# Kernel tuning notes

Hardware: AMD Instinct MI355X
Metric: run time of the kernel (lower is better)

Reference implementation:

```python
import jax, jax.numpy as jnp
import numpy as np

B, T, K = 128, 512, 256  # batch, seq_len, num_tags


def setup_inputs() -> dict:
    key = jax.random.key(0)
    k1, k2, k3 = jax.random.split(key, 3)
    y_pred = jax.random.normal(k1, (B, T, K), dtype=jnp.float32)
    trans = jax.random.normal(k2, (K, K), dtype=jnp.float32)
    y_true = jax.random.randint(k3, (B, T), 0, K)
    return {"y_pred": y_pred, "trans": trans, "y_true": y_true}


def reference(y_pred, trans, y_true):
    # sparse_loss: one-hot the integer labels
    num_tags = trans.shape[0]
    y_oh = jax.nn.one_hot(y_true, num_tags, dtype=y_pred.dtype)  # [B,T,K]

    # dense_loss: mask frames where all logits <= -1e6
    mask = jnp.all(y_pred > -1e6, axis=2, keepdims=True).astype(y_pred.dtype)  # [B,T,1]
    y_oh = y_oh * mask
    yp = y_pred * mask

    # target_score: emission score + transition score along the gold path
    point_score = jnp.einsum('bti,bti->b', y_oh, yp)
    trans_score = jnp.einsum('bti,ij,btj->b', y_oh[:, :-1], trans, y_oh[:, 1:])
    target_score = point_score + trans_score  # [B]

    # log_norm_step: forward algorithm (log-semiring recurrence) via scan
    init = yp[:, 0]  # [B,K]

    def step(alpha, xm):
        x, m = xm  # x: [B,K] emissions at t, m: [B,1] mask at t
        # logsumexp over previous tag: alpha[b,i] + trans[i,j]
        new = jax.nn.logsumexp(alpha[:, :, None] + trans[None, :, :], axis=1) + x
        alpha = m * new + (1.0 - m) * alpha
        return alpha, None

    xs = (jnp.swapaxes(yp[:, 1:], 0, 1), jnp.swapaxes(mask[:, 1:], 0, 1))  # time-major
    last_alpha, _ = jax.lax.scan(step, init, xs)  # [B,K]
    log_norm = jax.nn.logsumexp(last_alpha, axis=1)  # [B]

    return log_norm - target_score  # per-example CRF negative log-likelihood [B]
```

## Files before the change

kernel.cpp:

```cpp
#include <hip/hip_runtime.h>
#include <stdint.h>

#define T_ 512
#define K_ 256
#define NB 16
#define L2E 1.4426950408889634f
#define LN2 0.6931471805599453f

typedef __attribute__((ext_vector_type(8))) short short8;
typedef __attribute__((ext_vector_type(4))) float f32x4;

__device__ __forceinline__ float fexp2(float x) {
#if __has_builtin(__builtin_amdgcn_exp2f)
  return __builtin_amdgcn_exp2f(x);
#else
  return exp2f(x);
#endif
}
__device__ __forceinline__ float flog2(float x) {
#if __has_builtin(__builtin_amdgcn_logf)
  return __builtin_amdgcn_logf(x);
#else
  return log2f(x);
#endif
}
__device__ __forceinline__ unsigned int umax_(unsigned int a, unsigned int b) {
  return a > b ? a : b;
}
__device__ __forceinline__ unsigned short f2bf(float f) {
  union { float f; uint32_t u; } v; v.f = f;
  uint32_t r = v.u + 0x7fffu + ((v.u >> 16) & 1u);
  return (unsigned short)(r >> 16);
}

#define BAR() do { \
  asm volatile("s_waitcnt lgkmcnt(0)" ::: "memory"); \
  __builtin_amdgcn_s_barrier(); \
  asm volatile("" ::: "memory"); \
} while (0)


__global__ void prep_E(const float* __restrict__ trans, unsigned short* __restrict__ Efrag) {
  int idx = blockIdx.x * 256 + threadIdx.x;
  int e = idx & 7;
  int ln = (idx >> 3) & 63;
  int kb = (idx >> 9) & 7;
  int mt = idx >> 12;
  int j = mt * 16 + (ln & 15);
  int k = kb * 32 + ((ln >> 4) << 3) + e;
  Efrag[idx] = f2bf(__expf(trans[k * K_ + j]));
}

__global__ void aux_mask(const float* __restrict__ yp, unsigned char* __restrict__ masks) {
  int item = blockIdx.x * 4 + (threadIdx.x >> 6);
  int lane = threadIdx.x & 63;
  const float4 v = *(const float4*)(yp + (size_t)item * K_ + lane * 4);
  float mn = fminf(fminf(v.x, v.y), fminf(v.z, v.w));
  unsigned long long bl = __ballot(mn > -1000000.0f);
  if (lane == 0) {
    int b = item >> 9, t = item & 511;
    masks[t * 128 + b] = (bl == ~0ull) ? 1 : 0;
  }
}

__global__ void aux_score(const float* __restrict__ yp, const float* __restrict__ trans,
                          const int* __restrict__ ytrue, const unsigned char* __restrict__ masks,
                          float* __restrict__ score) {
  int b = blockIdx.x;
  int lane = threadIdx.x;
  float s = 0.f;
  #pragma unroll
  for (int k = 0; k < 8; ++k) {
    int t = lane + 64 * k;
    int y = ytrue[b * T_ + t];
    int m = masks[t * 128 + b];
    float x = yp[((size_t)b * T_ + t) * K_ + y];
    if (m) s += x;
    if (t >= 1) {
      int ym = ytrue[b * T_ + t - 1];
      int mm = masks[(t - 1) * 128 + b];
      if (m && mm) s += trans[ym * K_ + y];
    }
  }
  #pragma unroll
  for (int off = 32; off; off >>= 1) s += __shfl_xor(s, off, 64);
  if (lane == 0) score[b] = s;
}


template<int TM4, bool RESC, bool MWR, bool MASKED>
__device__ __forceinline__ void crf_step(
    int t, int c, int g, int wv, int swz, const int* tb,
    const short8 (&Ef)[4][8],
    float (&a)[16], float (&exf)[16], int& acc, int& mkc,
    const float* xb, float4 (&XN)[4], float4 (&XI)[4],
    unsigned short (*Wl)[NB * K_], const unsigned char* mkl, unsigned int* Mpart) {
  BAR();
  if (RESC) {
    unsigned int Mx = Mpart[c];
    Mx = umax_(Mx, Mpart[NB + c]);
    Mx = umax_(Mx, Mpart[2 * NB + c]);
    Mx = umax_(Mx, Mpart[3 * NB + c]);
    unsigned int e_ = Mx >> 23;
    float sf = __builtin_bit_cast(float, (254u - e_) << 23);
    if (!MASKED || mkc) acc += 127 - (int)e_;
    #pragma unroll
    for (int j = 0; j < 16; ++j) exf[j] *= sf;
  }
  f32x4 ac0 = {0.f, 0.f, 0.f, 0.f}, ac1 = {0.f, 0.f, 0.f, 0.f};
  f32x4 ac2 = {0.f, 0.f, 0.f, 0.f}, ac3 = {0.f, 0.f, 0.f, 0.f};
  {
    const unsigned short* rrow = &Wl[TM4 & 1][c * K_];
    #pragma unroll
    for (int kb = 0; kb < 8; ++kb) {
      short8 bf = __builtin_bit_cast(short8,
          *(const uint4*)(&rrow[(kb * 32 + g * 8) ^ swz]));
      ac0 = __builtin_amdgcn_mfma_f32_16x16x32_bf16(Ef[0][kb], bf, ac0, 0, 0, 0);
      ac1 = __builtin_amdgcn_mfma_f32_16x16x32_bf16(Ef[1][kb], bf, ac1, 0, 0, 0);
      ac2 = __builtin_amdgcn_mfma_f32_16x16x32_bf16(Ef[2][kb], bf, ac2, 0, 0, 0);
      ac3 = __builtin_amdgcn_mfma_f32_16x16x32_bf16(Ef[3][kb], bf, ac3, 0, 0, 0);
    }
  }
  if (MASKED) {
    #pragma unroll
    for (int i = 0; i < 4; ++i) { float an = ac0[i] * exf[i];      a[i]      = mkc ? an : a[i]; }
    #pragma unroll
    for (int i = 0; i < 4; ++i) { float an = ac1[i] * exf[4 + i];  a[4 + i]  = mkc ? an : a[4 + i]; }
    #pragma unroll
    for (int i = 0; i < 4; ++i) { float an = ac2[i] * exf[8 + i];  a[8 + i]  = mkc ? an : a[8 + i]; }
    #pragma unroll
    for (int i = 0; i < 4; ++i) { float an = ac3[i] * exf[12 + i]; a[12 + i] = mkc ? an : a[12 + i]; }
  } else {
    #pragma unroll
    for (int i = 0; i < 4; ++i) a[i]      = ac0[i] * exf[i];
    #pragma unroll
    for (int i = 0; i < 4; ++i) a[4 + i]  = ac1[i] * exf[4 + i];
    #pragma unroll
    for (int i = 0; i < 4; ++i) a[8 + i]  = ac2[i] * exf[8 + i];
    #pragma unroll
    for (int i = 0; i < 4; ++i) a[12 + i] = ac3[i] * exf[12 + i];
  }
  {
    unsigned short* wrow = &Wl[(TM4 + 1) & 1][c * K_];
    #pragma unroll
    for (int m = 0; m < 4; ++m) {
      uint32_t p0 = __builtin_amdgcn_perm(
          __builtin_bit_cast(uint32_t, a[4 * m + 1]),
          __builtin_bit_cast(uint32_t, a[4 * m + 0]), 0x07060302u);
      uint32_t p1 = __builtin_amdgcn_perm(
          __builtin_bit_cast(uint32_t, a[4 * m + 3]),
          __builtin_bit_cast(uint32_t, a[4 * m + 2]), 0x07060302u);
      uint2 pp; pp.x = p0; pp.y = p1;
      *(uint2*)(&wrow[tb[m] ^ swz]) = pp;
    }
  }
  if (MWR) {
    unsigned int pm = __builtin_bit_cast(uint32_t, a[0]);
    #pragma unroll
    for (int j = 1; j < 16; ++j) pm = umax_(pm, __builtin_bit_cast(uint32_t, a[j]));
    pm = umax_(pm, (unsigned int)__shfl_xor((int)pm, 16, 64));
    pm = umax_(pm, (unsigned int)__shfl_xor((int)pm, 32, 64));
    if (g == 0) Mpart[wv * NB + c] = pm;
  }
  #pragma unroll
  for (int m = 0; m < 4; ++m) {
    exf[4 * m + 0] = fexp2(XN[m].x * L2E);
    exf[4 * m + 1] = fexp2(XN[m].y * L2E);
    exf[4 * m + 2] = fexp2(XN[m].z * L2E);
    exf[4 * m + 3] = fexp2(XN[m].w * L2E);
  }
  if (MASKED) mkc = mkl[(t + 1 < T_ ? t + 1 : 0) * NB + c];
  {
    int tt = t + 4;
    tt = tt > (T_ - 1) ? (T_ - 1) : tt;
    #pragma unroll
    for (int m = 0; m < 4; ++m)
      XI[m] = *(const float4*)(xb + (size_t)tt * K_ + tb[m]);
  }
}

template<bool MASKED>
__device__ __forceinline__ void scan_run(
    int tid, int c, int g, int wv, int swz, const int* tb, int b0,
    const short8 (&Ef)[4][8], const float* xb,
    float4 (&xinit)[4], float4 (&X0q)[4], float4 (&X1q)[4],
    float4 (&X2q)[4], float4 (&X3q)[4],
    unsigned short (*Wl)[NB * K_], const unsigned char* mkl,
    unsigned int* Mpart, float* Spart,
    const float* __restrict__ score, float* __restrict__ out) {
  float a[16], exf[16];
  int acc = 0;
  int mkc = 0;
  {
    int mk0 = MASKED ? mkl[c] : 1;
    #pragma unroll
    for (int m = 0; m < 4; ++m) {
      float e0 = fexp2(xinit[m].x * L2E);
      float e1 = fexp2(xinit[m].y * L2E);
      float e2 = fexp2(xinit[m].z * L2E);
      float e3 = fexp2(xinit[m].w * L2E);
      a[4 * m + 0] = (MASKED && !mk0) ? 1.0f : e0;
      a[4 * m + 1] = (MASKED && !mk0) ? 1.0f : e1;
      a[4 * m + 2] = (MASKED && !mk0) ? 1.0f : e2;
      a[4 * m + 3] = (MASKED && !mk0) ? 1.0f : e3;
    }
  }
  {
    unsigned short* wrow = &Wl[1][c * K_];
    #pragma unroll
    for (int m = 0; m < 4; ++m) {
      uint32_t p0 = __builtin_amdgcn_perm(
          __builtin_bit_cast(uint32_t, a[4 * m + 1]),
          __builtin_bit_cast(uint32_t, a[4 * m + 0]), 0x07060302u);
      uint32_t p1 = __builtin_amdgcn_perm(
          __builtin_bit_cast(uint32_t, a[4 * m + 3]),
          __builtin_bit_cast(uint32_t, a[4 * m + 2]), 0x07060302u);
      uint2 pp; pp.x = p0; pp.y = p1;
      *(uint2*)(&wrow[tb[m] ^ swz]) = pp;
    }
  }
  #pragma unroll
  for (int m = 0; m < 4; ++m) {
    exf[4 * m + 0] = fexp2(X1q[m].x * L2E);
    exf[4 * m + 1] = fexp2(X1q[m].y * L2E);
    exf[4 * m + 2] = fexp2(X1q[m].z * L2E);
    exf[4 * m + 3] = fexp2(X1q[m].w * L2E);
  }
  if (MASKED) mkc = mkl[NB + c];

  crf_step<1, false, false, MASKED>(1, c, g, wv, swz, tb, Ef, a, exf, acc, mkc, xb, X2q, X1q, Wl, mkl, Mpart);
  crf_step<2, false, false, MASKED>(2, c, g, wv, swz, tb, Ef, a, exf, acc, mkc, xb, X3q, X2q, Wl, mkl, Mpart);
  crf_step<3, false, true , MASKED>(3, c, g, wv, swz, tb, Ef, a, exf, acc, mkc, xb, X0q, X3q, Wl, mkl, Mpart);

  #pragma unroll 1
  for (int t0 = 4; t0 < T_; t0 += 4) {
    crf_step<0, true , false, MASKED>(t0,     c, g, wv, swz, tb, Ef, a, exf, acc, mkc, xb, X1q, X0q, Wl, mkl, Mpart);
    crf_step<1, false, false, MASKED>(t0 + 1, c, g, wv, swz, tb, Ef, a, exf, acc, mkc, xb, X2q, X1q, Wl, mkl, Mpart);
    crf_step<2, false, false, MASKED>(t0 + 2, c, g, wv, swz, tb, Ef, a, exf, acc, mkc, xb, X3q, X2q, Wl, mkl, Mpart);
    crf_step<3, false, true , MASKED>(t0 + 3, c, g, wv, swz, tb, Ef, a, exf, acc, mkc, xb, X0q, X3q, Wl, mkl, Mpart);
  }

  __syncthreads();
  {
    float ssum = 0.f;
    #pragma unroll
    for (int j = 0; j < 16; ++j) ssum += a[j];
    ssum += __shfl_xor(ssum, 16, 64);
    ssum += __shfl_xor(ssum, 32, 64);
    if (g == 0) Spart[wv * NB + c] = ssum;
  }
  __syncthreads();
  if (tid < NB) {
    float S = Spart[tid] + Spart[NB + tid] + Spart[2 * NB + tid] + Spart[3 * NB + tid];
    out[b0 + tid] = LN2 * (flog2(S) - (float)acc) - score[b0 + tid];
  }
}

__global__ __launch_bounds__(256, 1) void crf_scan(
    const float* __restrict__ yp, const unsigned short* __restrict__ Efrag,
    const unsigned char* __restrict__ masks, const float* __restrict__ score,
    float* __restrict__ out) {
  const int b0 = blockIdx.x * NB;
  const int tid = threadIdx.x;
  const int wv = tid >> 6, lane = tid & 63;
  const int c = lane & 15;
  const int g = lane >> 4;
  const int swz = (c & 7) << 3;

  __shared__ unsigned short Wl[2][NB * K_];
  __shared__ unsigned char mkl[T_ * NB];
  __shared__ unsigned int Mpart[4 * NB];
  __shared__ float Spart[4 * NB];
  __shared__ int sflag[4];

  short8 Ef[4][8];
  {
    const uint4* ep = (const uint4*)Efrag;
    #pragma unroll
    for (int m = 0; m < 4; ++m)
      #pragma unroll
      for (int kb = 0; kb < 8; ++kb)
        Ef[m][kb] = __builtin_bit_cast(short8, ep[((wv * 4 + m) * 8 + kb) * 64 + lane]);
  }

  uint4 md0, md1;
  {
    uint4* dst = (uint4*)mkl;
    md0 = *(const uint4*)(masks + (tid)*128 + b0);
    md1 = *(const uint4*)(masks + (tid + 256) * 128 + b0);
    dst[tid] = md0;
    dst[tid + 256] = md1;
  }

  const float* xb = yp + (size_t)(b0 + c) * T_ * K_;
  int tb[4];
  #pragma unroll
  for (int m = 0; m < 4; ++m) tb[m] = wv * 64 + m * 16 + g * 4;

  float4 xinit[4], X0q[4], X1q[4], X2q[4], X3q[4];
  #pragma unroll
  for (int m = 0; m < 4; ++m) xinit[m] = *(const float4*)(xb + tb[m]);
  #pragma unroll
  for (int m = 0; m < 4; ++m) X1q[m] = *(const float4*)(xb + 1 * K_ + tb[m]);
  #pragma unroll
  for (int m = 0; m < 4; ++m) X2q[m] = *(const float4*)(xb + 2 * K_ + tb[m]);
  #pragma unroll
  for (int m = 0; m < 4; ++m) X3q[m] = *(const float4*)(xb + 3 * K_ + tb[m]);
  #pragma unroll
  for (int m = 0; m < 4; ++m) X0q[m] = *(const float4*)(xb + 4 * K_ + tb[m]);

  {
    uint32_t w = md0.x & md0.y & md0.z & md0.w & md1.x & md1.y & md1.z & md1.w;
    unsigned long long bl = __ballot(w == 0x01010101u);
    if (lane == 0) sflag[wv] = (bl == ~0ull) ? 1 : 0;
  }
  __syncthreads();
  bool allm = sflag[0] && sflag[1] && sflag[2] && sflag[3];

  if (allm) {
    scan_run<false>(tid, c, g, wv, swz, tb, b0, Ef, xb, xinit, X0q, X1q, X2q, X3q,
                    Wl, mkl, Mpart, Spart, score, out);
  } else {
    scan_run<true>(tid, c, g, wv, swz, tb, b0, Ef, xb, xinit, X0q, X1q, X2q, X3q,
                   Wl, mkl, Mpart, Spart, score, out);
  }
}

extern "C" void kernel_launch(void* const* d_in, const int* in_sizes, int n_in,
                              void* d_out, int out_size, void* d_ws, size_t ws_size,
                              hipStream_t stream) {
  const float* yp = (const float*)d_in[0];
  const float* trans = (const float*)d_in[1];
  const int* ytrue = (const int*)d_in[2];
  float* out = (float*)d_out;

  unsigned short* Efrag = (unsigned short*)d_ws;
  unsigned char* masks = (unsigned char*)d_ws + 131072;
  float* score = (float*)((char*)d_ws + 131072 + 65536);

  prep_E<<<dim3(256), dim3(256), 0, stream>>>(trans, Efrag);
  aux_mask<<<dim3(16384), dim3(256), 0, stream>>>(yp, masks);
  aux_score<<<dim3(128), dim3(64), 0, stream>>>(yp, trans, ytrue, masks, score);
  crf_scan<<<dim3(8), dim3(256), 0, stream>>>(yp, Efrag, masks, score, out);
}
```

Baseline: 303.7 us.

## Split MFMA accumulation chains, pad LDS rows, use packed bf16 convert

The MFMA K-loop now accumulates into two independent sets of accumulators (kb 0-3 and 4-7) that are summed afterwards, which halves the dependent MFMA chain length on the serial recurrence. The LDS buffer drops its XOR swizzle in favour of a padded row stride of 264 to avoid bank conflicts. The truncating perm-based bf16 packing is replaced by the v_cvt_pk_bf16_f32 instruction, which rounds. s_setprio is raised around the MFMA block. Costs are extra accumulator registers and a few adds, plus a small change in rounding behaviour.

```diff
diff --git a/kernel.cpp b/kernel.cpp
--- a/kernel.cpp
+++ b/kernel.cpp
@@ -4,6 +4,7 @@
 #define T_ 512
 #define K_ 256
 #define NB 16
+#define WROW 264
 #define L2E 1.4426950408889634f
 #define LN2 0.6931471805599453f
 
@@ -31,6 +32,11 @@
   union { float f; uint32_t u; } v; v.f = f;
   uint32_t r = v.u + 0x7fffu + ((v.u >> 16) & 1u);
   return (unsigned short)(r >> 16);
+}
+__device__ __forceinline__ uint32_t cvt_pk_bf16(float a, float b) {
+  uint32_t d;
+  asm("v_cvt_pk_bf16_f32 %0, %1, %2" : "=v"(d) : "v"(a), "v"(b));
+  return d;
 }
 
 #define BAR() do { \
@@ -90,11 +96,11 @@
 
 template<int TM4, bool RESC, bool MWR, bool MASKED>
 __device__ __forceinline__ void crf_step(
-    int t, int c, int g, int wv, int swz, const int* tb,
+    int t, int c, int g, int wv, const int* tb,
     const short8 (&Ef)[4][8],
     float (&a)[16], float (&exf)[16], int& acc, int& mkc,
     const float* xb, float4 (&XN)[4], float4 (&XI)[4],
-    unsigned short (*Wl)[NB * K_], const unsigned char* mkl, unsigned int* Mpart) {
+    unsigned short (*Wl)[NB * WROW], const unsigned char* mkl, unsigned int* Mpart) {
   BAR();
   if (RESC) {
     unsigned int Mx = Mpart[c];
@@ -107,51 +113,53 @@
     #pragma unroll
     for (int j = 0; j < 16; ++j) exf[j] *= sf;
   }
-  f32x4 ac0 = {0.f, 0.f, 0.f, 0.f}, ac1 = {0.f, 0.f, 0.f, 0.f};
-  f32x4 ac2 = {0.f, 0.f, 0.f, 0.f}, ac3 = {0.f, 0.f, 0.f, 0.f};
-  {
-    const unsigned short* rrow = &Wl[TM4 & 1][c * K_];
-    #pragma unroll
-    for (int kb = 0; kb < 8; ++kb) {
-      short8 bf = __builtin_bit_cast(short8,
-          *(const uint4*)(&rrow[(kb * 32 + g * 8) ^ swz]));
-      ac0 = __builtin_amdgcn_mfma_f32_16x16x32_bf16(Ef[0][kb], bf, ac0, 0, 0, 0);
-      ac1 = __builtin_amdgcn_mfma_f32_16x16x32_bf16(Ef[1][kb], bf, ac1, 0, 0, 0);
-      ac2 = __builtin_amdgcn_mfma_f32_16x16x32_bf16(Ef[2][kb], bf, ac2, 0, 0, 0);
-      ac3 = __builtin_amdgcn_mfma_f32_16x16x32_bf16(Ef[3][kb], bf, ac3, 0, 0, 0);
-    }
+  f32x4 acA[4], acB[4];
+  #pragma unroll
+  for (int m = 0; m < 4; ++m) { acA[m] = (f32x4){0.f,0.f,0.f,0.f}; acB[m] = (f32x4){0.f,0.f,0.f,0.f}; }
+  {
+    const unsigned short* rrow = &Wl[TM4 & 1][c * WROW];
+    __builtin_amdgcn_s_setprio(1);
+    #pragma unroll
+    for (int kb = 0; kb < 4; ++kb) {
+      short8 bf = __builtin_bit_cast(short8, *(const uint4*)(&rrow[kb * 32 + g * 8]));
+      acA[0] = __builtin_amdgcn_mfma_f32_16x16x32_bf16(Ef[0][kb], bf, acA[0], 0, 0, 0);
+      acA[1] = __builtin_amdgcn_mfma_f32_16x16x32_bf16(Ef[1][kb], bf, acA[1], 0, 0, 0);
+      acA[2] = __builtin_amdgcn_mfma_f32_16x16x32_bf16(Ef[2][kb], bf, acA[2], 0, 0, 0);
+      acA[3] = __builtin_amdgcn_mfma_f32_16x16x32_bf16(Ef[3][kb], bf, acA[3], 0, 0, 0);
+    }
+    #pragma unroll
+    for (int kb = 4; kb < 8; ++kb) {
+      short8 bf = __builtin_bit_cast(short8, *(const uint4*)(&rrow[kb * 32 + g * 8]));
+      acB[0] = __builtin_amdgcn_mfma_f32_16x16x32_bf16(Ef[0][kb], bf, acB[0], 0, 0, 0);
+      acB[1] = __builtin_amdgcn_mfma_f32_16x16x32_bf16(Ef[1][kb], bf, acB[1], 0, 0, 0);
+      acB[2] = __builtin_amdgcn_mfma_f32_16x16x32_bf16(Ef[2][kb], bf, acB[2], 0, 0, 0);
+      acB[3] = __builtin_amdgcn_mfma_f32_16x16x32_bf16(Ef[3][kb], bf, acB[3], 0, 0, 0);
+    }
+    __builtin_amdgcn_s_setprio(0);
   }
   if (MASKED) {
     #pragma unroll
-    for (int i = 0; i < 4; ++i) { float an = ac0[i] * exf[i];      a[i]      = mkc ? an : a[i]; }
-    #pragma unroll
-    for (int i = 0; i < 4; ++i) { float an = ac1[i] * exf[4 + i];  a[4 + i]  = mkc ? an : a[4 + i]; }
-    #pragma unroll
-    for (int i = 0; i < 4; ++i) { float an = ac2[i] * exf[8 + i];  a[8 + i]  = mkc ? an : a[8 + i]; }
-    #pragma unroll
-    for (int i = 0; i < 4; ++i) { float an = ac3[i] * exf[12 + i]; a[12 + i] = mkc ? an : a[12 + i]; }
+    for (int m = 0; m < 4; ++m)
+      #pragma unroll
+      for (int i = 0; i < 4; ++i) {
+        float an = (acA[m][i] + acB[m][i]) * exf[4 * m + i];
+        a[4 * m + i] = mkc ? an : a[4 * m + i];
+      }
   } else {
     #pragma unroll
-    for (int i = 0; i < 4; ++i) a[i]      = ac0[i] * exf[i];
-    #pragma unroll
-    for (int i = 0; i < 4; ++i) a[4 + i]  = ac1[i] * exf[4 + i];
-    #pragma unroll
-    for (int i = 0; i < 4; ++i) a[8 + i]  = ac2[i] * exf[8 + i];
-    #pragma unroll
-    for (int i = 0; i < 4; ++i) a[12 + i] = ac3[i] * exf[12 + i];
-  }
-  {
-    unsigned short* wrow = &Wl[(TM4 + 1) & 1][c * K_];
+    for (int m = 0; m < 4; ++m)
+      #pragma unroll
+      for (int i = 0; i < 4; ++i)
+        a[4 * m + i] = (acA[m][i] + acB[m][i]) * exf[4 * m + i];
+  }
+  {
+    unsigned short* wrow = &Wl[(TM4 + 1) & 1][c * WROW];
     #pragma unroll
     for (int m = 0; m < 4; ++m) {
-      uint32_t p0 = __builtin_amdgcn_perm(
-          __builtin_bit_cast(uint32_t, a[4 * m + 1]),
-          __builtin_bit_cast(uint32_t, a[4 * m + 0]), 0x07060302u);
-      uint32_t p1 = __builtin_amdgcn_perm(
-          __builtin_bit_cast(uint32_t, a[4 * m + 3]),
-          __builtin_bit_cast(uint32_t, a[4 * m + 2]), 0x07060302u);
-      uint2 pp; pp.x = p0; pp.y = p1;
-      *(uint2*)(&wrow[tb[m] ^ swz]) = pp;
+      uint2 pp;
+      pp.x = cvt_pk_bf16(a[4 * m + 0], a[4 * m + 1]);
+      pp.y = cvt_pk_bf16(a[4 * m + 2], a[4 * m + 3]);
+      *(uint2*)(&wrow[tb[m]]) = pp;
     }
   }
   if (MWR) {
@@ -181,11 +189,11 @@
 
 template<bool MASKED>
 __device__ __forceinline__ void scan_run(
-    int tid, int c, int g, int wv, int swz, const int* tb, int b0,
+    int tid, int c, int g, int wv, const int* tb, int b0,
     const short8 (&Ef)[4][8], const float* xb,
     float4 (&xinit)[4], float4 (&X0q)[4], float4 (&X1q)[4],
     float4 (&X2q)[4], float4 (&X3q)[4],
-    unsigned short (*Wl)[NB * K_], const unsigned char* mkl,
+    unsigned short (*Wl)[NB * WROW], const unsigned char* mkl,
     unsigned int* Mpart, float* Spart,
     const float* __restrict__ score, float* __restrict__ out) {
   float a[16], exf[16];
@@ -206,17 +214,13 @@
     }
   }
   {
-    unsigned short* wrow = &Wl[1][c * K_];
+    unsigned short* wrow = &Wl[1][c * WROW];
     #pragma unroll
     for (int m = 0; m < 4; ++m) {
-      uint32_t p0 = __builtin_amdgcn_perm(
-          __builtin_bit_cast(uint32_t, a[4 * m + 1]),
-          __builtin_bit_cast(uint32_t, a[4 * m + 0]), 0x07060302u);
-      uint32_t p1 = __builtin_amdgcn_perm(
-          __builtin_bit_cast(uint32_t, a[4 * m + 3]),
-          __builtin_bit_cast(uint32_t, a[4 * m + 2]), 0x07060302u);
-      uint2 pp; pp.x = p0; pp.y = p1;
-      *(uint2*)(&wrow[tb[m] ^ swz]) = pp;
+      uint2 pp;
+      pp.x = cvt_pk_bf16(a[4 * m + 0], a[4 * m + 1]);
+      pp.y = cvt_pk_bf16(a[4 * m + 2], a[4 * m + 3]);
+      *(uint2*)(&wrow[tb[m]]) = pp;
     }
   }
   #pragma unroll
@@ -228,16 +232,16 @@
   }
   if (MASKED) mkc = mkl[NB + c];
 
-  crf_step<1, false, false, MASKED>(1, c, g, wv, swz, tb, Ef, a, exf, acc, mkc, xb, X2q, X1q, Wl, mkl, Mpart);
-  crf_step<2, false, false, MASKED>(2, c, g, wv, swz, tb, Ef, a, exf, acc, mkc, xb, X3q, X2q, Wl, mkl, Mpart);
-  crf_step<3, false, true , MASKED>(3, c, g, wv, swz, tb, Ef, a, exf, acc, mkc, xb, X0q, X3q, Wl, mkl, Mpart);
+  crf_step<1, false, false, MASKED>(1, c, g, wv, tb, Ef, a, exf, acc, mkc, xb, X2q, X1q, Wl, mkl, Mpart);
+  crf_step<2, false, false, MASKED>(2, c, g, wv, tb, Ef, a, exf, acc, mkc, xb, X3q, X2q, Wl, mkl, Mpart);
+  crf_step<3, false, true , MASKED>(3, c, g, wv, tb, Ef, a, exf, acc, mkc, xb, X0q, X3q, Wl, mkl, Mpart);
 
   #pragma unroll 1
   for (int t0 = 4; t0 < T_; t0 += 4) {
-    crf_step<0, true , false, MASKED>(t0,     c, g, wv, swz, tb, Ef, a, exf, acc, mkc, xb, X1q, X0q, Wl, mkl, Mpart);
-    crf_step<1, false, false, MASKED>(t0 + 1, c, g, wv, swz, tb, Ef, a, exf, acc, mkc, xb, X2q, X1q, Wl, mkl, Mpart);
-    crf_step<2, false, false, MASKED>(t0 + 2, c, g, wv, swz, tb, Ef, a, exf, acc, mkc, xb, X3q, X2q, Wl, mkl, Mpart);
-    crf_step<3, false, true , MASKED>(t0 + 3, c, g, wv, swz, tb, Ef, a, exf, acc, mkc, xb, X0q, X3q, Wl, mkl, Mpart);
+    crf_step<0, true , false, MASKED>(t0,     c, g, wv, tb, Ef, a, exf, acc, mkc, xb, X1q, X0q, Wl, mkl, Mpart);
+    crf_step<1, false, false, MASKED>(t0 + 1, c, g, wv, tb, Ef, a, exf, acc, mkc, xb, X2q, X1q, Wl, mkl, Mpart);
+    crf_step<2, false, false, MASKED>(t0 + 2, c, g, wv, tb, Ef, a, exf, acc, mkc, xb, X3q, X2q, Wl, mkl, Mpart);
+    crf_step<3, false, true , MASKED>(t0 + 3, c, g, wv, tb, Ef, a, exf, acc, mkc, xb, X0q, X3q, Wl, mkl, Mpart);
   }
 
   __syncthreads();
@@ -265,9 +269,8 @@
   const int wv = tid >> 6, lane = tid & 63;
   const int c = lane & 15;
   const int g = lane >> 4;
-  const int swz = (c & 7) << 3;
-
-  __shared__ unsigned short Wl[2][NB * K_];
+
+  __shared__ unsigned short Wl[2][NB * WROW];
   __shared__ unsigned char mkl[T_ * NB];
   __shared__ unsigned int Mpart[4 * NB];
   __shared__ float Spart[4 * NB];
@@ -318,10 +321,10 @@
   bool allm = sflag[0] && sflag[1] && sflag[2] && sflag[3];
 
   if (allm) {
-    scan_run<false>(tid, c, g, wv, swz, tb, b0, Ef, xb, xinit, X0q, X1q, X2q, X3q,
+    scan_run<false>(tid, c, g, wv, tb, b0, Ef, xb, xinit, X0q, X1q, X2q, X3q,
                     Wl, mkl, Mpart, Spart, score, out);
   } else {
-    scan_run<true>(tid, c, g, wv, swz, tb, b0, Ef, xb, xinit, X0q, X1q, X2q, X3q,
+    scan_run<true>(tid, c, g, wv, tb, b0, Ef, xb, xinit, X0q, X1q, X2q, X3q,
                    Wl, mkl, Mpart, Spart, score, out);
   }
 }
```

Measured after the change: 374.0 us. 1.23x slower.
